# Optimization experiments

Hardware: AMD Instinct MI355X
Metric: run time of the kernel (lower is better)

Reference implementation:

```python
import jax, jax.numpy as jnp
import numpy as np

HEADS = 4
HEAD_DIM = 32  # hidden_dim // num_heads = 128 // 4
HIDDEN = 128
NEG_SLOPE = 0.2  # GATConv default


def gat_conv(x, src, dst, W, att_src, att_dst, bias):
    """PyG GATConv (concat=True, default negative_slope=0.2), eval mode.
    x: [N, F_in], src/dst: [E] (self-loops already included)."""
    N = x.shape[0]
    h = (x @ W).reshape(N, HEADS, HEAD_DIM)               # [N, H, D]
    a_src = jnp.einsum('nhd,hd->nh', h, att_src)          # [N, H]
    a_dst = jnp.einsum('nhd,hd->nh', h, att_dst)
    e = jax.nn.leaky_relu(a_src[src] + a_dst[dst], NEG_SLOPE)  # [E, H]
    # numerically stable softmax over incoming edges of each dst node
    m = jax.ops.segment_max(e, dst, num_segments=N)
    m = jnp.where(jnp.isfinite(m), m, 0.0)
    p = jnp.exp(e - m[dst])
    denom = jax.ops.segment_sum(p, dst, num_segments=N)
    alpha = p / (denom[dst] + 1e-16)                      # [E, H]
    out = jax.ops.segment_sum(h[src] * alpha[..., None], dst, num_segments=N)
    return out.reshape(N, HEADS * HEAD_DIM) + bias


def setup_inputs() -> dict:
    key = jax.random.key(0)
    ks = jax.random.split(key, 20)
    n_news, n_tweets, E = 20000, 80000, 1600000
    N = n_news + n_tweets
    s = 0.05
    inp = {
        'x_news': jax.random.normal(ks[0], (n_news, 768), jnp.float32),
        'x_tweets': jax.random.normal(ks[1], (n_tweets, 512), jnp.float32),
        'edge_index': jax.random.randint(ks[2], (2, E), 0, N, jnp.int32),
        'W_news': jax.random.normal(ks[3], (768, HIDDEN), jnp.float32) * s,
        'b_news': jnp.zeros((HIDDEN,), jnp.float32),
        'W_tw': jax.random.normal(ks[4], (512, HIDDEN), jnp.float32) * s,
        'b_tw': jnp.zeros((HIDDEN,), jnp.float32),
        'gat1_W': jax.random.normal(ks[5], (HIDDEN, HIDDEN), jnp.float32) * s,
        'gat1_as': jax.random.normal(ks[6], (HEADS, HEAD_DIM), jnp.float32) * s,
        'gat1_ad': jax.random.normal(ks[7], (HEADS, HEAD_DIM), jnp.float32) * s,
        'gat1_b': jnp.zeros((HIDDEN,), jnp.float32),
        'gat2_W': jax.random.normal(ks[8], (HIDDEN, HIDDEN), jnp.float32) * s,
        'gat2_as': jax.random.normal(ks[9], (HEADS, HEAD_DIM), jnp.float32) * s,
        'gat2_ad': jax.random.normal(ks[10], (HEADS, HEAD_DIM), jnp.float32) * s,
        'gat2_b': jnp.zeros((HIDDEN,), jnp.float32),
        'Wc1': jax.random.normal(ks[11], (HIDDEN, HIDDEN // 2), jnp.float32) * s,
        'bc1': jnp.zeros((HIDDEN // 2,), jnp.float32),
        'Wc2': jax.random.normal(ks[12], (HIDDEN // 2, 2), jnp.float32) * s,
        'bc2': jnp.zeros((2,), jnp.float32),
    }
    return inp


def reference(x_news, x_tweets, edge_index, W_news, b_news, W_tw, b_tw,
              gat1_W, gat1_as, gat1_ad, gat1_b,
              gat2_W, gat2_as, gat2_ad, gat2_b,
              Wc1, bc1, Wc2, bc2):
    n_news = x_news.shape[0]
    # encoders (dropout is identity in eval)
    h_news = jax.nn.relu(x_news @ W_news + b_news)
    h_tw = jax.nn.relu(x_tweets @ W_tw + b_tw)
    x = jnp.concatenate([h_news, h_tw], axis=0)           # [N, 128]
    N = x.shape[0]
    # GATConv default: add self-loops
    loops = jnp.arange(N, dtype=edge_index.dtype)
    src = jnp.concatenate([edge_index[0], loops])
    dst = jnp.concatenate([edge_index[1], loops])
    x = jax.nn.elu(gat_conv(x, src, dst, gat1_W, gat1_as, gat1_ad, gat1_b))
    x = jax.nn.elu(gat_conv(x, src, dst, gat2_W, gat2_as, gat2_ad, gat2_b))
    news_emb = x[:n_news]
    out = jax.nn.relu(news_emb @ Wc1 + bc1) @ Wc2 + bc2   # [n_news, 2]
    return out
```

## Files before the change

### kernel.cpp

```cpp
#include <hip/hip_runtime.h>
#include <hip/hip_bf16.h>
#include <type_traits>

typedef __attribute__((ext_vector_type(8))) short bf16x8;
typedef __attribute__((ext_vector_type(8))) unsigned short u16x8;
typedef __attribute__((ext_vector_type(4))) float f32x4;

__device__ __forceinline__ unsigned short f2b(float f) {
  union { float f; unsigned u; } c; c.f = f;
  return (unsigned short)((c.u + 0x7fffu + ((c.u >> 16) & 1u)) >> 16);
}
__device__ __forceinline__ float b2f(unsigned short v) {
  return __uint_as_float((unsigned)v << 16);
}

template<int BM, int K, int BKT, int ACT, int LOGITS, typename AT>
__device__ __forceinline__ void gemm_body(
    int bid, unsigned short* As,
    const AT* __restrict__ A, int M,
    const unsigned short* __restrict__ WT, const float* __restrict__ bias,
    unsigned short* __restrict__ C,
    const float* __restrict__ att_src, const float* __restrict__ att_dst,
    float* __restrict__ a_src, float* __restrict__ a_dst)
{
  constexpr int LSW = BKT + 8;
  constexpr int MF = BM / 16;
  constexpr int NF = 2;
  const int t = threadIdx.x;
  const int lane = t & 63;
  const int wc = t >> 6;
  const int fr = lane & 15;
  const int kb = lane >> 4;
  const long row0 = (long)bid * BM;

  f32x4 acc[MF][NF] = {};

  for (int k0 = 0; k0 < K; k0 += BKT) {
    if constexpr (std::is_same<AT, float>::value) {
      constexpr int NU = BM * (BKT / 4) / 256;
      float4 rv[NU];
#pragma unroll
      for (int i = 0; i < NU; ++i) {
        int idx = t + i * 256;
        int r = idx / (BKT / 4);
        int kq = idx % (BKT / 4);
        long gr = row0 + r; if (gr >= M) gr = M - 1;
        rv[i] = *(const float4*)(A + gr * K + k0 + kq * 4);
      }
#pragma unroll
      for (int i = 0; i < NU; ++i) {
        int idx = t + i * 256;
        int r = idx / (BKT / 4);
        int kq = idx % (BKT / 4);
        ushort4 b;
        b.x = f2b(rv[i].x); b.y = f2b(rv[i].y); b.z = f2b(rv[i].z); b.w = f2b(rv[i].w);
        *(ushort4*)(&As[r * LSW + kq * 4]) = b;
      }
    } else {
      constexpr int NU = BM * (BKT / 8) / 256;
      u16x8 rv[NU];
#pragma unroll
      for (int i = 0; i < NU; ++i) {
        int idx = t + i * 256;
        int r = idx / (BKT / 8);
        int k8 = idx % (BKT / 8);
        long gr = row0 + r; if (gr >= M) gr = M - 1;
        rv[i] = *(const u16x8*)(A + gr * K + k0 + k8 * 8);
      }
#pragma unroll
      for (int i = 0; i < NU; ++i) {
        int idx = t + i * 256;
        int r = idx / (BKT / 8);
        int k8 = idx % (BKT / 8);
        *(u16x8*)(&As[r * LSW + k8 * 8]) = rv[i];
      }
    }
    __syncthreads();
#pragma unroll
    for (int kk = 0; kk < BKT; kk += 32) {
      const int koff = kk + kb * 8;
      bf16x8 af[MF], bfr[NF];
#pragma unroll
      for (int n = 0; n < NF; ++n)
        bfr[n] = *(const bf16x8*)(WT + (long)(wc * 32 + n * 16 + fr) * K + k0 + koff);
#pragma unroll
      for (int m = 0; m < MF; ++m)
        af[m] = *(const bf16x8*)(&As[(m * 16 + fr) * LSW + koff]);
#pragma unroll
      for (int m = 0; m < MF; ++m)
#pragma unroll
        for (int n = 0; n < NF; ++n)
          acc[m][n] = __builtin_amdgcn_mfma_f32_16x16x32_bf16(af[m], bfr[n], acc[m][n], 0, 0, 0);
    }
    if (k0 + BKT < K) __syncthreads();
  }

  float asv[NF], adv[NF];
  if (LOGITS) {
#pragma unroll
    for (int n = 0; n < NF; ++n) {
      int dim = n * 16 + fr;
      asv[n] = att_src[wc * 32 + dim];
      adv[n] = att_dst[wc * 32 + dim];
    }
  }

#pragma unroll
  for (int m = 0; m < MF; ++m) {
#pragma unroll
    for (int j = 0; j < 4; ++j) {
      long gr = row0 + m * 16 + kb * 4 + j;
      if (gr < M) {
#pragma unroll
        for (int n = 0; n < NF; ++n) {
          int c = wc * 32 + n * 16 + fr;
          float v = acc[m][n][j];
          if (bias) v += bias[c];
          if (ACT == 1) v = fmaxf(v, 0.f);
          C[gr * 128 + c] = f2b(v);
        }
      }
      if (LOGITS) {
        float sa = fmaf(acc[m][0][j], asv[0], acc[m][1][j] * asv[1]);
        float da = fmaf(acc[m][0][j], adv[0], acc[m][1][j] * adv[1]);
#pragma unroll
        for (int off = 1; off < 16; off <<= 1) {
          sa += __shfl_xor(sa, off);
          da += __shfl_xor(da, off);
        }
        if (fr == 0 && gr < M) {
          a_src[gr * 4 + wc] = sa;
          a_dst[gr * 4 + wc] = da;
        }
      }
    }
  }
}

__device__ __forceinline__ void hist_body(int bid, int* cnt, const int* __restrict__ dst,
                                          int E, int* __restrict__ bcount, int nb)
{
  int t = threadIdx.x;
  for (int b = t; b < 512; b += 256) cnt[b] = 0;
  __syncthreads();
  int e0 = bid * 8192;
  for (int i = 0; i < 32; ++i) {
    int e = e0 + i * 256 + t;
    if (e < E) atomicAdd(&cnt[dst[e] >> 8], 1);
  }
  __syncthreads();
  for (int b = t; b < nb; b += 256) {
    int c = cnt[b];
    if (c > 0) atomicAdd(&bcount[b], c);
  }
}

__device__ __forceinline__ void scatter_body(int bid, int* s, const int* __restrict__ src,
                                             const int* __restrict__ dst, int E,
                                             int* __restrict__ bcur, int2* __restrict__ pairs)
{
  int* cnt = s;
  int* base = s + 512;
  int* rcur = s + 1024;
  int t = threadIdx.x;
  for (int b = t; b < 512; b += 256) { cnt[b] = 0; rcur[b] = 0; }
  __syncthreads();
  int e0 = bid * 8192;
  for (int i = 0; i < 32; ++i) {
    int e = e0 + i * 256 + t;
    if (e < E) atomicAdd(&cnt[dst[e] >> 8], 1);
  }
  __syncthreads();
  for (int b = t; b < 512; b += 256) {
    int c = cnt[b];
    if (c > 0) base[b] = atomicAdd(&bcur[b], c);
  }
  __syncthreads();
  for (int i = 0; i < 32; ++i) {
    int e = e0 + i * 256 + t;
    if (e < E) {
      int d = dst[e];
      int b = d >> 8;
      int off = atomicAdd(&rcur[b], 1);
      int2 p; p.x = src[e]; p.y = d;
      pairs[base[b] + off] = p;
    }
  }
}

__global__ __launch_bounds__(256) void mega1_kernel(
    int nb_tw, int nb_news,
    const float* __restrict__ x_tw, int n_tw, const unsigned short* __restrict__ WT_tw,
    const float* __restrict__ b_tw, unsigned short* __restrict__ out_tw,
    const float* __restrict__ x_news, int n_news, const unsigned short* __restrict__ WT_news,
    const float* __restrict__ b_news, unsigned short* __restrict__ out_news,
    const int* __restrict__ dst, int E, int* __restrict__ bcount, int nb)
{
  __shared__ unsigned short sh[64 * (256 + 8)];
  int bid = blockIdx.x;
  if (bid < nb_tw) {
    gemm_body<64, 512, 256, 1, 0, float>(bid, sh, x_tw, n_tw, WT_tw, b_tw, out_tw,
                                         nullptr, nullptr, nullptr, nullptr);
  } else if (bid < nb_tw + nb_news) {
    gemm_body<32, 768, 256, 1, 0, float>(bid - nb_tw, sh, x_news, n_news, WT_news,
                                         b_news, out_news, nullptr, nullptr, nullptr, nullptr);
  } else {
    hist_body(bid - nb_tw - nb_news, (int*)sh, dst, E, bcount, nb);
  }
}

__global__ __launch_bounds__(256) void mega3_kernel(
    int nb_gemm,
    const unsigned short* __restrict__ x_feat, int N, const unsigned short* __restrict__ WT_g1,
    unsigned short* __restrict__ h_feat,
    const float* __restrict__ g1as, const float* __restrict__ g1ad,
    float* __restrict__ a_src, float* __restrict__ a_dst,
    const int* __restrict__ src, const int* __restrict__ dst, int E,
    int* __restrict__ bcur, int2* __restrict__ pairs)
{
  __shared__ unsigned short sh[64 * (128 + 8)];
  int bid = blockIdx.x;
  if (bid < nb_gemm) {
    gemm_body<64, 128, 128, 0, 1, unsigned short>(bid, sh, x_feat, N, WT_g1, nullptr,
                                                  h_feat, g1as, g1ad, a_src, a_dst);
  } else {
    scatter_body(bid - nb_gemm, (int*)sh, src, dst, E, bcur, pairs);
  }
}

template<int BM, int K, int BKT, int ACT, int LOGITS, typename AT>
__global__ __launch_bounds__(256) void gemm_kernel(
    const AT* __restrict__ A, int M,
    const unsigned short* __restrict__ WT, const float* __restrict__ bias,
    unsigned short* __restrict__ C,
    const float* __restrict__ att_src, const float* __restrict__ att_dst,
    float* __restrict__ a_src, float* __restrict__ a_dst)
{
  __shared__ unsigned short sh[BM * (BKT + 8)];
  gemm_body<BM, K, BKT, ACT, LOGITS, AT>(blockIdx.x, sh, A, M, WT, bias, C,
                                         att_src, att_dst, a_src, a_dst);
}

__global__ void transpose_all_kernel(const float* __restrict__ W0, unsigned short* __restrict__ T0,
                                     const float* __restrict__ W1, unsigned short* __restrict__ T1,
                                     const float* __restrict__ W2, unsigned short* __restrict__ T2,
                                     const float* __restrict__ W3, unsigned short* __restrict__ T3)
{
  int r = blockIdx.x * 256 + threadIdx.x;
  if (r < 128 * 768) { int c = r / 768, k = r - c * 768; T0[r] = f2b(W0[(size_t)k * 128 + c]); return; }
  r -= 128 * 768;
  if (r < 128 * 512) { int c = r / 512, k = r - c * 512; T1[r] = f2b(W1[(size_t)k * 128 + c]); return; }
  r -= 128 * 512;
  if (r < 128 * 128) { T2[r] = f2b(W2[(size_t)(r & 127) * 128 + (r >> 7)]); return; }
  r -= 128 * 128;
  if (r < 128 * 128) { T3[r] = f2b(W3[(size_t)(r & 127) * 128 + (r >> 7)]); return; }
}

__global__ __launch_bounds__(512) void bucket_scan_kernel(const int* __restrict__ bcount, int nb, int E,
                                                          int* __restrict__ bstart, int* __restrict__ bcur,
                                                          int* __restrict__ row_ptr, int N)
{
  __shared__ int s[512];
  int t = threadIdx.x;
  int my = (t < nb) ? bcount[t] : 0;
  s[t] = my;
  __syncthreads();
  for (int off = 1; off < 512; off <<= 1) {
    int v = (t >= off) ? s[t - off] : 0;
    __syncthreads();
    s[t] += v;
    __syncthreads();
  }
  int excl = s[t] - my;
  if (t < nb) { bstart[t] = excl; bcur[t] = excl; }
  if (t == 0) { bstart[nb] = E; row_ptr[N] = E; }
}

__global__ __launch_bounds__(256) void bucket_csr_kernel(const int2* __restrict__ pairs,
                                                         const int* __restrict__ bstart, int N,
                                                         int* __restrict__ row_ptr, int* __restrict__ col_idx)
{
  __shared__ int cnt[256];
  __shared__ int excl[256];
  __shared__ int cur[256];
  int t = threadIdx.x;
  int nodebase = blockIdx.x << 8;
  int start = bstart[blockIdx.x];
  int size = bstart[blockIdx.x + 1] - start;
  cnt[t] = 0;
  __syncthreads();
  for (int i = t; i < size; i += 256)
    atomicAdd(&cnt[pairs[start + i].y & 255], 1);
  __syncthreads();
  int my = cnt[t];
  excl[t] = my;
  __syncthreads();
  for (int off = 1; off < 256; off <<= 1) {
    int v = (t >= off) ? excl[t - off] : 0;
    __syncthreads();
    excl[t] += v;
    __syncthreads();
  }
  int ex = excl[t] - my;
  if (nodebase + t < N) row_ptr[nodebase + t] = start + ex;
  excl[t] = ex;
  cur[t] = 0;
  __syncthreads();
  for (int i = t; i < size; i += 256) {
    int2 p = pairs[start + i];
    int local = p.y & 255;
    int pos = start + excl[local] + atomicAdd(&cur[local], 1);
    col_idx[pos] = p.x;
  }
}

__global__ void gat_aggregate_kernel(const unsigned short* __restrict__ h, const float* __restrict__ a_src,
                                     const float* __restrict__ a_dst, const int* __restrict__ row_ptr,
                                     const int* __restrict__ col_idx, const float* __restrict__ bias,
                                     int Nproc, unsigned short* __restrict__ out)
{
  int n = (blockIdx.x * blockDim.x + threadIdx.x) >> 6;
  int lane = threadIdx.x & 63;
  if (n >= Nproc) return;
  const int sub = lane >> 4;
  const int sl = lane & 15;
  const int head = sl >> 2;
  const int beg = row_ptr[n], end = row_ptr[n + 1];
  const float adst = a_dst[(size_t)n * 4 + head];

  float slf = a_src[(size_t)n * 4 + head] + adst;
  slf = fmaxf(slf, 0.2f * slf);
  float ps = (sub == 0) ? __expf(slf) : 0.f;
  float denom = ps;
  float acc[8];
  {
    const u16x8 hs = *(const u16x8*)(h + (size_t)n * 128 + 8 * sl);
#pragma unroll
    for (int j = 0; j < 8; ++j) acc[j] = ps * b2f(hs[j]);
  }

  int e = beg + sub;
  for (; e + 4 < end; e += 8) {
    const int s0 = col_idx[e];
    const int s1 = col_idx[e + 4];
    const u16x8 h0 = *(const u16x8*)(h + (size_t)s0 * 128 + 8 * sl);
    const u16x8 h1 = *(const u16x8*)(h + (size_t)s1 * 128 + 8 * sl);
    float l0 = a_src[(size_t)s0 * 4 + head] + adst;
    float l1 = a_src[(size_t)s1 * 4 + head] + adst;
    l0 = fmaxf(l0, 0.2f * l0);
    l1 = fmaxf(l1, 0.2f * l1);
    const float p0 = __expf(l0);
    const float p1 = __expf(l1);
    denom += p0 + p1;
#pragma unroll
    for (int j = 0; j < 8; ++j) {
      acc[j] = fmaf(p0, b2f(h0[j]), acc[j]);
      acc[j] = fmaf(p1, b2f(h1[j]), acc[j]);
    }
  }
  if (e < end) {
    const int s = col_idx[e];
    const u16x8 hv = *(const u16x8*)(h + (size_t)s * 128 + 8 * sl);
    float lg = a_src[(size_t)s * 4 + head] + adst;
    lg = fmaxf(lg, 0.2f * lg);
    const float p = __expf(lg);
    denom += p;
#pragma unroll
    for (int j = 0; j < 8; ++j) acc[j] = fmaf(p, b2f(hv[j]), acc[j]);
  }

#pragma unroll
  for (int j = 0; j < 8; ++j) {
    acc[j] += __shfl_xor(acc[j], 16);
    acc[j] += __shfl_xor(acc[j], 32);
  }
  denom += __shfl_xor(denom, 16);
  denom += __shfl_xor(denom, 32);

  if (sub == 0) {
    const float inv = 1.0f / (denom + 1e-16f);
    const float4 b0 = *(const float4*)(bias + 8 * sl);
    const float4 b1 = *(const float4*)(bias + 8 * sl + 4);
    float o[8];
    o[0] = acc[0] * inv + b0.x; o[1] = acc[1] * inv + b0.y;
    o[2] = acc[2] * inv + b0.z; o[3] = acc[3] * inv + b0.w;
    o[4] = acc[4] * inv + b1.x; o[5] = acc[5] * inv + b1.y;
    o[6] = acc[6] * inv + b1.z; o[7] = acc[7] * inv + b1.w;
    u16x8 r;
#pragma unroll
    for (int j = 0; j < 8; ++j) {
      float v = (o[j] > 0.f) ? o[j] : expm1f(o[j]);
      r[j] = f2b(v);
    }
    *(u16x8*)(out + (size_t)n * 128 + 8 * sl) = r;
  }
}

__global__ void gat_agg_cls_kernel(const unsigned short* __restrict__ h, const float* __restrict__ a_src,
                                   const float* __restrict__ a_dst, const int* __restrict__ row_ptr,
                                   const int* __restrict__ col_idx, const float* __restrict__ bias,
                                   int n_news,
                                   const float* __restrict__ Wc1, const float* __restrict__ bc1,
                                   const float* __restrict__ Wc2, const float* __restrict__ bc2,
                                   float* __restrict__ out)
{
  int n = (blockIdx.x * blockDim.x + threadIdx.x) >> 6;
  int lane = threadIdx.x & 63;
  if (n >= n_news) return;
  const int sub = lane >> 4;
  const int sl = lane & 15;
  const int head = sl >> 2;
  const int beg = row_ptr[n], end = row_ptr[n + 1];
  const float adst = a_dst[(size_t)n * 4 + head];

  float slf = a_src[(size_t)n * 4 + head] + adst;
  slf = fmaxf(slf, 0.2f * slf);
  float ps = (sub == 0) ? __expf(slf) : 0.f;
  float denom = ps;
  float acc[8];
  {
    const u16x8 hs = *(const u16x8*)(h + (size_t)n * 128 + 8 * sl);
#pragma unroll
    for (int j = 0; j < 8; ++j) acc[j] = ps * b2f(hs[j]);
  }

  int e = beg + sub;
  for (; e + 4 < end; e += 8) {
    const int s0 = col_idx[e];
    const int s1 = col_idx[e + 4];
    const u16x8 h0 = *(const u16x8*)(h + (size_t)s0 * 128 + 8 * sl);
    const u16x8 h1 = *(const u16x8*)(h + (size_t)s1 * 128 + 8 * sl);
    float l0 = a_src[(size_t)s0 * 4 + head] + adst;
    float l1 = a_src[(size_t)s1 * 4 + head] + adst;
    l0 = fmaxf(l0, 0.2f * l0);
    l1 = fmaxf(l1, 0.2f * l1);
    const float p0 = __expf(l0);
    const float p1 = __expf(l1);
    denom += p0 + p1;
#pragma unroll
    for (int j = 0; j < 8; ++j) {
      acc[j] = fmaf(p0, b2f(h0[j]), acc[j]);
      acc[j] = fmaf(p1, b2f(h1[j]), acc[j]);
    }
  }
  if (e < end) {
    const int s = col_idx[e];
    const u16x8 hv = *(const u16x8*)(h + (size_t)s * 128 + 8 * sl);
    float lg = a_src[(size_t)s * 4 + head] + adst;
    lg = fmaxf(lg, 0.2f * lg);
    const float p = __expf(lg);
    denom += p;
#pragma unroll
    for (int j = 0; j < 8; ++j) acc[j] = fmaf(p, b2f(hv[j]), acc[j]);
  }

#pragma unroll
  for (int j = 0; j < 8; ++j) {
    acc[j] += __shfl_xor(acc[j], 16);
    acc[j] += __shfl_xor(acc[j], 32);
  }
  denom += __shfl_xor(denom, 16);
  denom += __shfl_xor(denom, 32);

  const float inv = 1.0f / (denom + 1e-16f);
  const float4 b0 = *(const float4*)(bias + 8 * sl);
  const float4 b1 = *(const float4*)(bias + 8 * sl + 4);
  float o[8];
  o[0] = acc[0] * inv + b0.x; o[1] = acc[1] * inv + b0.y;
  o[2] = acc[2] * inv + b0.z; o[3] = acc[3] * inv + b0.w;
  o[4] = acc[4] * inv + b1.x; o[5] = acc[5] * inv + b1.y;
  o[6] = acc[6] * inv + b1.z; o[7] = acc[7] * inv + b1.w;
#pragma unroll
  for (int j = 0; j < 8; ++j)
    o[j] = (o[j] > 0.f) ? o[j] : expm1f(o[j]);

  float c = 0.f;
#pragma unroll
  for (int j = 0; j < 8; ++j) {
#pragma unroll
    for (int kb = 0; kb < 16; ++kb) {
      float x = __shfl(o[j], kb);
      c = fmaf(x, Wc1[(kb * 8 + j) * 64 + lane], c);
    }
  }
  c += bc1[lane];
  c = fmaxf(c, 0.f);
  float o0 = c * Wc2[lane * 2 + 0];
  float o1 = c * Wc2[lane * 2 + 1];
#pragma unroll
  for (int off = 1; off < 64; off <<= 1) {
    o0 += __shfl_xor(o0, off);
    o1 += __shfl_xor(o1, off);
  }
  if (lane == 0) {
    out[(size_t)n * 2 + 0] = o0 + bc2[0];
    out[(size_t)n * 2 + 1] = o1 + bc2[1];
  }
}

extern "C" void kernel_launch(void* const* d_in, const int* in_sizes, int n_in,
                              void* d_out, int out_size, void* d_ws, size_t ws_size,
                              hipStream_t stream)
{
  const float* x_news = (const float*)d_in[0];
  const float* x_tw   = (const float*)d_in[1];
  const int*   ei     = (const int*)d_in[2];
  const float* W_news = (const float*)d_in[3];
  const float* b_news = (const float*)d_in[4];
  const float* W_tw   = (const float*)d_in[5];
  const float* b_tw   = (const float*)d_in[6];
  const float* g1W  = (const float*)d_in[7];
  const float* g1as = (const float*)d_in[8];
  const float* g1ad = (const float*)d_in[9];
  const float* g1b  = (const float*)d_in[10];
  const float* g2W  = (const float*)d_in[11];
  const float* g2as = (const float*)d_in[12];
  const float* g2ad = (const float*)d_in[13];
  const float* g2b  = (const float*)d_in[14];
  const float* Wc1  = (const float*)d_in[15];
  const float* bc1  = (const float*)d_in[16];
  const float* Wc2  = (const float*)d_in[17];
  const float* bc2  = (const float*)d_in[18];

  const int n_news = in_sizes[0] / 768;
  const int n_tw   = in_sizes[1] / 512;
  const int N = n_news + n_tw;
  const int E = in_sizes[2] / 2;
  const int* src = ei;
  const int* dst = ei + E;
  const int nb = (N + 255) >> 8;

  char* ws = (char*)d_ws;
  size_t off = 0;
  auto alloc = [&](size_t bytes) -> void* {
    void* p = ws + off;
    off += (bytes + 255) & ~(size_t)255;
    return p;
  };
  unsigned short* x_feat = (unsigned short*)alloc((size_t)N * 128 * 2);
  unsigned short* h_feat = (unsigned short*)alloc((size_t)N * 128 * 2);
  float* a_src   = (float*)alloc((size_t)N * 4 * 4);
  float* a_dst   = (float*)alloc((size_t)N * 4 * 4);
  int*   row_ptr = (int*)alloc((size_t)(N + 1) * 4);
  int*   col_idx = (int*)alloc((size_t)E * 4);
  int2*  pairs   = (int2*)alloc((size_t)E * 8);
  int*   bcount  = (int*)alloc(2048);
  int*   bstart  = (int*)alloc(2052);
  int*   bcur    = (int*)alloc(2048);
  unsigned short* WT_news = (unsigned short*)alloc((size_t)128 * 768 * 2);
  unsigned short* WT_tw   = (unsigned short*)alloc((size_t)128 * 512 * 2);
  unsigned short* WT_g1   = (unsigned short*)alloc((size_t)128 * 128 * 2);
  unsigned short* WT_g2   = (unsigned short*)alloc((size_t)128 * 128 * 2);

  hipMemsetAsync(bcount, 0, 2048, stream);

  transpose_all_kernel<<<768, 256, 0, stream>>>(W_news, WT_news, W_tw, WT_tw, g1W, WT_g1, g2W, WT_g2);

  const int nb_tw = (n_tw + 63) / 64;
  const int nb_news = (n_news + 31) / 32;
  const int nb_hist = (E + 8191) / 8192;
  mega1_kernel<<<nb_tw + nb_news + nb_hist, 256, 0, stream>>>(
      nb_tw, nb_news,
      x_tw, n_tw, WT_tw, b_tw, x_feat + (size_t)n_news * 128,
      x_news, n_news, WT_news, b_news, x_feat,
      dst, E, bcount, nb);

  bucket_scan_kernel<<<1, 512, 0, stream>>>(bcount, nb, E, bstart, bcur, row_ptr, N);

  const int nb_g = (N + 63) / 64;
  mega3_kernel<<<nb_g + nb_hist, 256, 0, stream>>>(
      nb_g, x_feat, N, WT_g1, h_feat, g1as, g1ad, a_src, a_dst,
      src, dst, E, bcur, pairs);

  bucket_csr_kernel<<<nb, 256, 0, stream>>>(pairs, bstart, N, row_ptr, col_idx);

  gat_aggregate_kernel<<<(N + 3) / 4, 256, 0, stream>>>(h_feat, a_src, a_dst, row_ptr, col_idx, g1b, N, x_feat);

  gemm_kernel<64, 128, 128, 0, 1, unsigned short><<<nb_g, 256, 0, stream>>>(
      x_feat, N, WT_g2, nullptr, h_feat, g2as, g2ad, a_src, a_dst);
  gat_agg_cls_kernel<<<(n_news + 3) / 4, 256, 0, stream>>>(
      h_feat, a_src, a_dst, row_ptr, col_idx, g2b, n_news,
      Wc1, bc1, Wc2, bc2, (float*)d_out);
}
```

Before: 341.2 us.

## Stage weight tiles in LDS and shrink GEMM K-tile to 64

The GEMM body now cooperatively loads a 128x64 tile of the transposed weight matrix into shared memory each K-step, instead of having every wave read weight fragments straight from global memory. The K tile shrinks from 256/128 to 64 so that the A and B tiles fit in a smaller shared buffer. This is meant to cut redundant global and L2 traffic for the weights and to reduce LDS footprint, which could raise occupancy. In exchange there are more K iterations, each with two barriers, and the load-all-then-store register staging is removed, so less memory latency is hidden per iteration.

Result: faster. 307.5 us (-9.9%).

```diff
diff --git a/kernel.cpp b/kernel.cpp
--- a/kernel.cpp
+++ b/kernel.cpp
@@ -14,92 +14,85 @@
   return __uint_as_float((unsigned)v << 16);
 }
 
-template<int BM, int K, int BKT, int ACT, int LOGITS, typename AT>
+constexpr int BK = 64;
+constexpr int LS = BK + 8;
+
+template<int BM, int K, int ACT, int LOGITS, typename AT>
 __device__ __forceinline__ void gemm_body(
-    int bid, unsigned short* As,
+    int bid, unsigned short* As, unsigned short* Bs,
     const AT* __restrict__ A, int M,
     const unsigned short* __restrict__ WT, const float* __restrict__ bias,
     unsigned short* __restrict__ C,
     const float* __restrict__ att_src, const float* __restrict__ att_dst,
     float* __restrict__ a_src, float* __restrict__ a_dst)
 {
-  constexpr int LSW = BKT + 8;
+  constexpr int WTN = 32;
   constexpr int MF = BM / 16;
   constexpr int NF = 2;
   const int t = threadIdx.x;
   const int lane = t & 63;
   const int wc = t >> 6;
-  const int fr = lane & 15;
-  const int kb = lane >> 4;
   const long row0 = (long)bid * BM;
 
   f32x4 acc[MF][NF] = {};
 
-  for (int k0 = 0; k0 < K; k0 += BKT) {
+  for (int k0 = 0; k0 < K; k0 += BK) {
     if constexpr (std::is_same<AT, float>::value) {
-      constexpr int NU = BM * (BKT / 4) / 256;
-      float4 rv[NU];
-#pragma unroll
-      for (int i = 0; i < NU; ++i) {
+#pragma unroll
+      for (int i = 0; i < BM / 16; ++i) {
         int idx = t + i * 256;
-        int r = idx / (BKT / 4);
-        int kq = idx % (BKT / 4);
+        int r = idx >> 4;
+        int kq = idx & 15;
         long gr = row0 + r; if (gr >= M) gr = M - 1;
-        rv[i] = *(const float4*)(A + gr * K + k0 + kq * 4);
-      }
-#pragma unroll
-      for (int i = 0; i < NU; ++i) {
-        int idx = t + i * 256;
-        int r = idx / (BKT / 4);
-        int kq = idx % (BKT / 4);
+        const float4 v = *(const float4*)(A + gr * K + k0 + kq * 4);
         ushort4 b;
-        b.x = f2b(rv[i].x); b.y = f2b(rv[i].y); b.z = f2b(rv[i].z); b.w = f2b(rv[i].w);
-        *(ushort4*)(&As[r * LSW + kq * 4]) = b;
+        b.x = f2b(v.x); b.y = f2b(v.y); b.z = f2b(v.z); b.w = f2b(v.w);
+        *(ushort4*)(&As[r * LS + kq * 4]) = b;
       }
     } else {
-      constexpr int NU = BM * (BKT / 8) / 256;
-      u16x8 rv[NU];
-#pragma unroll
-      for (int i = 0; i < NU; ++i) {
+#pragma unroll
+      for (int i = 0; i < BM / 32; ++i) {
         int idx = t + i * 256;
-        int r = idx / (BKT / 8);
-        int k8 = idx % (BKT / 8);
+        int r = idx >> 3;
+        int k8 = idx & 7;
         long gr = row0 + r; if (gr >= M) gr = M - 1;
-        rv[i] = *(const u16x8*)(A + gr * K + k0 + k8 * 8);
+        u16x8 v = *(const u16x8*)(A + gr * K + k0 + k8 * 8);
+        *(u16x8*)(&As[r * LS + k8 * 8]) = v;
       }
-#pragma unroll
-      for (int i = 0; i < NU; ++i) {
-        int idx = t + i * 256;
-        int r = idx / (BKT / 8);
-        int k8 = idx % (BKT / 8);
-        *(u16x8*)(&As[r * LSW + k8 * 8]) = rv[i];
-      }
+    }
+#pragma unroll
+    for (int i = 0; i < 4; ++i) {
+      int idx = t + i * 256;
+      int col = idx >> 3;
+      int k8 = idx & 7;
+      u16x8 v = *(const u16x8*)(WT + (long)col * K + k0 + k8 * 8);
+      *(u16x8*)(&Bs[col * LS + k8 * 8]) = v;
     }
     __syncthreads();
 #pragma unroll
-    for (int kk = 0; kk < BKT; kk += 32) {
-      const int koff = kk + kb * 8;
+    for (int kk = 0; kk < BK; kk += 32) {
+      const int koff = kk + (lane >> 4) * 8;
       bf16x8 af[MF], bfr[NF];
 #pragma unroll
       for (int n = 0; n < NF; ++n)
-        bfr[n] = *(const bf16x8*)(WT + (long)(wc * 32 + n * 16 + fr) * K + k0 + koff);
+        bfr[n] = *(const bf16x8*)(&Bs[(wc * WTN + n * 16 + (lane & 15)) * LS + koff]);
 #pragma unroll
       for (int m = 0; m < MF; ++m)
-        af[m] = *(const bf16x8*)(&As[(m * 16 + fr) * LSW + koff]);
+        af[m] = *(const bf16x8*)(&As[(m * 16 + (lane & 15)) * LS + koff]);
 #pragma unroll
       for (int m = 0; m < MF; ++m)
 #pragma unroll
         for (int n = 0; n < NF; ++n)
           acc[m][n] = __builtin_amdgcn_mfma_f32_16x16x32_bf16(af[m], bfr[n], acc[m][n], 0, 0, 0);
     }
-    if (k0 + BKT < K) __syncthreads();
+    __syncthreads();
   }
 
   float asv[NF], adv[NF];
   if (LOGITS) {
 #pragma unroll
     for (int n = 0; n < NF; ++n) {
-      int dim = n * 16 + fr;
+      int dim = n * 16 + (lane & 15);
       asv[n] = att_src[wc * 32 + dim];
       adv[n] = att_dst[wc * 32 + dim];
     }
@@ -109,11 +102,11 @@
   for (int m = 0; m < MF; ++m) {
 #pragma unroll
     for (int j = 0; j < 4; ++j) {
-      long gr = row0 + m * 16 + kb * 4 + j;
+      long gr = row0 + m * 16 + (lane >> 4) * 4 + j;
       if (gr < M) {
 #pragma unroll
         for (int n = 0; n < NF; ++n) {
-          int c = wc * 32 + n * 16 + fr;
+          int c = wc * WTN + n * 16 + (lane & 15);
           float v = acc[m][n][j];
           if (bias) v += bias[c];
           if (ACT == 1) v = fmaxf(v, 0.f);
@@ -128,7 +121,7 @@
           sa += __shfl_xor(sa, off);
           da += __shfl_xor(da, off);
         }
-        if (fr == 0 && gr < M) {
+        if ((lane & 15) == 0 && gr < M) {
           a_src[gr * 4 + wc] = sa;
           a_dst[gr * 4 + wc] = da;
         }
@@ -196,14 +189,14 @@
     const float* __restrict__ b_news, unsigned short* __restrict__ out_news,
     const int* __restrict__ dst, int E, int* __restrict__ bcount, int nb)
 {
-  __shared__ unsigned short sh[64 * (256 + 8)];
+  __shared__ unsigned short sh[(64 + 128) * LS];
   int bid = blockIdx.x;
   if (bid < nb_tw) {
-    gemm_body<64, 512, 256, 1, 0, float>(bid, sh, x_tw, n_tw, WT_tw, b_tw, out_tw,
-                                         nullptr, nullptr, nullptr, nullptr);
+    gemm_body<64, 512, 1, 0, float>(bid, sh, sh + 64 * LS, x_tw, n_tw, WT_tw, b_tw, out_tw,
+                                    nullptr, nullptr, nullptr, nullptr);
   } else if (bid < nb_tw + nb_news) {
-    gemm_body<32, 768, 256, 1, 0, float>(bid - nb_tw, sh, x_news, n_news, WT_news,
-                                         b_news, out_news, nullptr, nullptr, nullptr, nullptr);
+    gemm_body<32, 768, 1, 0, float>(bid - nb_tw, sh, sh + 32 * LS, x_news, n_news, WT_news,
+                                    b_news, out_news, nullptr, nullptr, nullptr, nullptr);
   } else {
     hist_body(bid - nb_tw - nb_news, (int*)sh, dst, E, bcount, nb);
   }
@@ -218,17 +211,17 @@
     const int* __restrict__ src, const int* __restrict__ dst, int E,
     int* __restrict__ bcur, int2* __restrict__ pairs)
 {
-  __shared__ unsigned short sh[64 * (128 + 8)];
+  __shared__ unsigned short sh[(64 + 128) * LS];
   int bid = blockIdx.x;
   if (bid < nb_gemm) {
-    gemm_body<64, 128, 128, 0, 1, unsigned short>(bid, sh, x_feat, N, WT_g1, nullptr,
-                                                  h_feat, g1as, g1ad, a_src, a_dst);
+    gemm_body<64, 128, 0, 1, unsigned short>(bid, sh, sh + 64 * LS, x_feat, N, WT_g1, nullptr,
+                                             h_feat, g1as, g1ad, a_src, a_dst);
   } else {
     scatter_body(bid - nb_gemm, (int*)sh, src, dst, E, bcur, pairs);
   }
 }
 
-template<int BM, int K, int BKT, int ACT, int LOGITS, typename AT>
+template<int BM, int K, int ACT, int LOGITS, typename AT>
 __global__ __launch_bounds__(256) void gemm_kernel(
     const AT* __restrict__ A, int M,
     const unsigned short* __restrict__ WT, const float* __restrict__ bias,
@@ -236,9 +229,9 @@
     const float* __restrict__ att_src, const float* __restrict__ att_dst,
     float* __restrict__ a_src, float* __restrict__ a_dst)
 {
-  __shared__ unsigned short sh[BM * (BKT + 8)];
-  gemm_body<BM, K, BKT, ACT, LOGITS, AT>(blockIdx.x, sh, A, M, WT, bias, C,
-                                         att_src, att_dst, a_src, a_dst);
+  __shared__ unsigned short sh[(BM + 128) * LS];
+  gemm_body<BM, K, ACT, LOGITS, AT>(blockIdx.x, sh, sh + BM * LS, A, M, WT, bias, C,
+                                    att_src, att_dst, a_src, a_dst);
 }
 
 __global__ void transpose_all_kernel(const float* __restrict__ W0, unsigned short* __restrict__ T0,
@@ -576,7 +569,7 @@
 
   gat_aggregate_kernel<<<(N + 3) / 4, 256, 0, stream>>>(h_feat, a_src, a_dst, row_ptr, col_idx, g1b, N, x_feat);
 
-  gemm_kernel<64, 128, 128, 0, 1, unsigned short><<<nb_g, 256, 0, stream>>>(
+  gemm_kernel<64, 128, 0, 1, unsigned short><<<nb_g, 256, 0, stream>>>(
       x_feat, N, WT_g2, nullptr, h_feat, g2as, g2ad, a_src, a_dst);
   gat_agg_cls_kernel<<<(n_news + 3) / 4, 256, 0, stream>>>(
       h_feat, a_src, a_dst, row_ptr, col_idx, g2b, n_news,
```
